# Kernel tuning notes

Hardware: AMD Instinct MI355X
Metric: run time of the kernel (lower is better)

The kernel has to match this reference:

```python
import jax, jax.numpy as jnp
import numpy as np
import math

H = 1024
N_HEADS = 16
B, S = 2, 2048

def setup_inputs() -> dict:
    key = jax.random.key(0)
    ks = jax.random.split(key, 10)
    s = 0.02
    inp = {
        "x": jax.random.normal(ks[0], (B, S, H), dtype=jnp.float32),
        "attention_mask": jnp.zeros((B, 1, 1, S), dtype=jnp.float32),
        "Wq": jax.random.normal(ks[1], (H, H), dtype=jnp.float32) * s,
        "bq": jnp.zeros((H,), dtype=jnp.float32),
        "Wk": jax.random.normal(ks[2], (H, H), dtype=jnp.float32) * s,
        "bk": jnp.zeros((H,), dtype=jnp.float32),
        "Wv": jax.random.normal(ks[3], (H, H), dtype=jnp.float32) * s,
        "bv": jnp.zeros((H,), dtype=jnp.float32),
        "Wo": jax.random.normal(ks[4], (H, H), dtype=jnp.float32) * s,
        "bo": jnp.zeros((H,), dtype=jnp.float32),
    }
    return inp

def reference(x, attention_mask, Wq, bq, Wk, bk, Wv, bv, Wo, bo):
    b, s, h = x.shape
    n = N_HEADS
    d = h // n
    scale = 1.0 / math.sqrt(h / n)
    # Linear projections (torch Linear: x @ W.T + b)
    q = (x @ Wq.T + bq).reshape(b, s, n, d).transpose(0, 2, 1, 3)  # [b,n,s,d]
    k = (x @ Wk.T + bk).reshape(b, s, n, d).transpose(0, 2, 1, 3)
    v = (x @ Wv.T + bv).reshape(b, s, n, d).transpose(0, 2, 1, 3)
    scores = jnp.einsum("bnqd,bnkd->bnqk", q, k) * scale + attention_mask
    probs = jax.nn.softmax(scores, axis=-1)
    attn = jnp.einsum("bnqk,bnkd->bnqd", probs, v)
    attn = attn.transpose(0, 2, 1, 3).reshape(b, s, h)
    return attn @ Wo.T + bo
```

## Files before the change

### kernel.cpp

```cpp
#include <hip/hip_runtime.h>

typedef __bf16 bf16;
typedef __bf16 bf16x8 __attribute__((ext_vector_type(8)));
typedef __bf16 bf16x4 __attribute__((ext_vector_type(4)));
typedef float f32x4 __attribute__((ext_vector_type(4)));
typedef unsigned int u32;
typedef const u32 __attribute__((address_space(1)))* gp1_t;
typedef u32 __attribute__((address_space(3)))* lp3_t;

constexpr int Hdim = 1024;
constexpr int SEQ  = 2048;
constexpr int NB   = 2;
constexpr int NHEAD = 16;
constexpr int DHEAD = 64;
constexpr int MR = NB * SEQ;
constexpr float LOG2E = 1.4426950408889634f;
constexpr float QSCALE = 0.125f * LOG2E;

__device__ __forceinline__ float fexp2(float x) { return __builtin_amdgcn_exp2f(x); }

__device__ __forceinline__ void gld16(const void* g, void* l) {
  __builtin_amdgcn_global_load_lds((gp1_t)g, (lp3_t)l, 16, 0, 0);
}

__global__ __launch_bounds__(256) void cvt_all_k(
    const float* __restrict__ x, const float* __restrict__ Wq, const float* __restrict__ Wk,
    const float* __restrict__ Wv, const float* __restrict__ Wo, const float* __restrict__ mask,
    bf16* __restrict__ xb, bf16* __restrict__ wqkv, bf16* __restrict__ wob,
    float* __restrict__ maskS) {
  const int n8x = MR * Hdim / 8;
  const int n8w = Hdim * Hdim / 8;
  int i = blockIdx.x * 256 + threadIdx.x;
  if (i >= n8x + 4 * n8w) {
    int o = i - (n8x + 4 * n8w);
    const float4* p = reinterpret_cast<const float4*>(mask) + (size_t)o * 2;
    float4 a = p[0], b = p[1];
    a.x *= LOG2E; a.y *= LOG2E; a.z *= LOG2E; a.w *= LOG2E;
    b.x *= LOG2E; b.y *= LOG2E; b.z *= LOG2E; b.w *= LOG2E;
    float4* q = reinterpret_cast<float4*>(maskS) + (size_t)o * 2;
    q[0] = a; q[1] = b;
    return;
  }
  const float* src;
  bf16* dst;
  int slot;
  if (i < n8x) {
    src = x; dst = xb; slot = i;
  } else {
    int j = i - n8x;
    int w = j >> 17;
    int o = j & (n8w - 1);
    if (w == 0)      { src = Wq; dst = wqkv;            }
    else if (w == 1) { src = Wk; dst = wqkv + (size_t)Hdim * Hdim;     }
    else if (w == 2) { src = Wv; dst = wqkv + (size_t)2 * Hdim * Hdim; }
    else             { src = Wo; dst = wob;             }
    slot = o;
  }
  const float4* p = reinterpret_cast<const float4*>(src) + (size_t)slot * 2;
  float4 a = p[0], b = p[1];
  bf16x8 o8;
  o8[0] = (bf16)a.x; o8[1] = (bf16)a.y; o8[2] = (bf16)a.z; o8[3] = (bf16)a.w;
  o8[4] = (bf16)b.x; o8[5] = (bf16)b.y; o8[6] = (bf16)b.z; o8[7] = (bf16)b.w;
  reinterpret_cast<bf16x8*>(dst)[slot] = o8;
}

__global__ __launch_bounds__(256) void qkv_gemm_k(
    const bf16* __restrict__ A, const bf16* __restrict__ Bw,
    const float* __restrict__ bq, const float* __restrict__ bk, const float* __restrict__ bv,
    bf16* __restrict__ Qw, bf16* __restrict__ Kw, bf16* __restrict__ VTw)
{
  __shared__ __align__(16) bf16 As[3][128][32];
  __shared__ __align__(16) bf16 Bs[3][128][32];

  const int t = threadIdx.x;
  const int lane = t & 63, wave = t >> 6;
  const int ql = lane & 15, g = lane >> 4;
  const int wr = wave >> 1, wc = wave & 1;
  const int row0 = blockIdx.x * 128;
  const int col0 = blockIdx.y * 128;
  const int z = blockIdx.y >> 3;
  const float* bias = (z == 0) ? bq : (z == 1) ? bk : bv;

  f32x4 acc[4][4] = {};

#define STAGE_QKV(buf, kt)                                                        \
  {                                                                               \
    _Pragma("unroll")                                                             \
    for (int i = 0; i < 2; ++i) {                                                 \
      int c = i * 256 + t;                                                        \
      int r = c >> 2, o = (c & 3) << 3;                                           \
      gld16(&A[(size_t)(row0 + r) * Hdim + (kt) + o], (char*)&As[buf][0][0] + c * 16); \
      gld16(&Bw[(size_t)(col0 + r) * Hdim + (kt) + o], (char*)&Bs[buf][0][0] + c * 16); \
    }                                                                             \
  }

  constexpr int NT = Hdim / 32;
  STAGE_QKV(0, 0);
  STAGE_QKV(1, 32);

  int cur = 0;
  for (int it = 0; it < NT; ++it) {
    if (it + 2 < NT) {
      int stg = cur + 2; if (stg >= 3) stg -= 3;
      STAGE_QKV(stg, (it + 2) * 32);
      asm volatile("s_waitcnt vmcnt(8)" ::: "memory");
    } else if (it + 1 < NT) {
      asm volatile("s_waitcnt vmcnt(4)" ::: "memory");
    } else {
      asm volatile("s_waitcnt vmcnt(0)" ::: "memory");
    }
    __builtin_amdgcn_s_barrier();

    bf16x8 af[4], bfr[4];
#pragma unroll
    for (int m = 0; m < 4; ++m)
      af[m] = *reinterpret_cast<const bf16x8*>(&As[cur][wr * 64 + m * 16 + ql][g * 8]);
#pragma unroll
    for (int n = 0; n < 4; ++n)
      bfr[n] = *reinterpret_cast<const bf16x8*>(&Bs[cur][wc * 64 + n * 16 + ql][g * 8]);
#pragma unroll
    for (int m = 0; m < 4; ++m)
#pragma unroll
      for (int n = 0; n < 4; ++n)
        acc[m][n] = __builtin_amdgcn_mfma_f32_16x16x32_bf16(af[m], bfr[n], acc[m][n], 0, 0, 0);

    __builtin_amdgcn_s_barrier();
    cur = (cur + 1 == 3) ? 0 : cur + 1;
  }
#undef STAGE_QKV

  const float oscale = (z == 0) ? QSCALE : 1.0f;
#pragma unroll
  for (int m = 0; m < 4; ++m) {
#pragma unroll
    for (int n = 0; n < 4; ++n) {
#pragma unroll
      for (int r = 0; r < 4; ++r) {
        int gi = row0 + wr * 64 + m * 16 + g * 4 + r;
        int gj = col0 + wc * 64 + n * 16 + ql;
        int j1 = gj & (Hdim - 1);
        float v = (acc[m][n][r] + bias[j1]) * oscale;
        int b = gi >> 11, s = gi & (SEQ - 1);
        int hh = j1 >> 6, dd = j1 & 63;
        if (z == 0)
          Qw[((size_t)(b * NHEAD + hh) * SEQ + s) * DHEAD + dd] = (bf16)v;
        else if (z == 1)
          Kw[((size_t)(b * NHEAD + hh) * SEQ + s) * DHEAD + dd] = (bf16)v;
        else
          VTw[((size_t)(b * NHEAD + hh) * DHEAD + dd) * SEQ + s] = (bf16)v;
      }
    }
  }
}

__global__ __launch_bounds__(256, 2) void attn_fwd_k(
    const bf16* __restrict__ Q, const bf16* __restrict__ K,
    const bf16* __restrict__ VT, const float* __restrict__ maskS,
    bf16* __restrict__ Out)
{
  const int head = blockIdx.x;
  const int qt = blockIdx.y;
  const int b = head >> 4;
  const int hh = head & 15;
  const int t = threadIdx.x, lane = t & 63, wave = t >> 6;
  const int ql = lane & 15, g = lane >> 4;
  const int swz = (ql & 7) << 4;

  __shared__ __align__(16) bf16 Ks[2][64][64];
  __shared__ __align__(16) bf16 VTs[2][64][64];
  __shared__ __align__(16) bf16 Ps[4][32][64];

  const bf16* Qh  = Q  + (size_t)head * SEQ * DHEAD;
  const bf16* Kh  = K  + (size_t)head * SEQ * DHEAD;
  const bf16* VTh = VT + (size_t)head * DHEAD * SEQ;
  const float* mrow = maskS + (size_t)b * SEQ;

  const int q0w = qt * 128 + wave * 32;
  char* psw = (char*)&Ps[wave][0][0];

  bf16x8 qf[2][2];
#pragma unroll
  for (int qm = 0; qm < 2; ++qm)
#pragma unroll
    for (int kk = 0; kk < 2; ++kk)
      qf[qm][kk] = *reinterpret_cast<const bf16x8*>(
          &Qh[(size_t)(q0w + qm * 16 + ql) * DHEAD + kk * 32 + g * 8]);

  f32x4 accT[2][4] = {};
  f32x4 psum4[2] = {{0.f, 0.f, 0.f, 0.f}, {0.f, 0.f, 0.f, 0.f}};

#pragma unroll
  for (int i = 0; i < 2; ++i) {
    int c = i * 256 + t, r = c >> 3, sp = c & 7, sl = sp ^ (r & 7);
    gld16(&Kh[(size_t)r * DHEAD + sl * 8], (char*)&Ks[0][0][0] + c * 16);
    gld16(&VTh[(size_t)r * SEQ + sl * 8], (char*)&VTs[0][0][0] + c * 16);
  }
  __syncthreads();

  for (int it = 0; it < SEQ / 64; ++it) {
    const int cur = it & 1;
    const int kb0 = it * 64;

    f32x4 mk4[4];
#pragma unroll
    for (int kb = 0; kb < 4; ++kb)
      mk4[kb] = *reinterpret_cast<const f32x4*>(mrow + kb0 + kb * 16 + g * 4);

    if (it + 1 < SEQ / 64) {
      const int nb0 = kb0 + 64;
#pragma unroll
      for (int i = 0; i < 2; ++i) {
        int c = i * 256 + t, r = c >> 3, sp = c & 7, sl = sp ^ (r & 7);
        gld16(&Kh[(size_t)(nb0 + r) * DHEAD + sl * 8], (char*)&Ks[cur ^ 1][0][0] + c * 16);
        gld16(&VTh[(size_t)r * SEQ + nb0 + sl * 8], (char*)&VTs[cur ^ 1][0][0] + c * 16);
      }
    }

    const char* ksb = (const char*)&Ks[cur][0][0];
    const char* vsb = (const char*)&VTs[cur][0][0];

    bf16x8 kf[4][2];
#pragma unroll
    for (int kb = 0; kb < 4; ++kb) {
      const int row = kb * 16 + ql;
#pragma unroll
      for (int kk = 0; kk < 2; ++kk)
        kf[kb][kk] = *reinterpret_cast<const bf16x8*>(ksb + row * 128 + ((kk * 64 + g * 16) ^ swz));
    }
    f32x4 sacc[2][4];
#pragma unroll
    for (int qm = 0; qm < 2; ++qm)
#pragma unroll
      for (int kb = 0; kb < 4; ++kb) sacc[qm][kb] = mk4[kb];
    __builtin_amdgcn_s_setprio(1);
#pragma unroll
    for (int qm = 0; qm < 2; ++qm)
#pragma unroll
      for (int kb = 0; kb < 4; ++kb)
#pragma unroll
        for (int kk = 0; kk < 2; ++kk)
          sacc[qm][kb] = __builtin_amdgcn_mfma_f32_16x16x32_bf16(kf[kb][kk], qf[qm][kk], sacc[qm][kb], 0, 0, 0);
    __builtin_amdgcn_s_setprio(0);

#pragma unroll
    for (int qm = 0; qm < 2; ++qm) {
      const int qrow = qm * 16 + ql;
#pragma unroll
      for (int kb = 0; kb < 2; ++kb) {
        bf16x4 p4;
        f32x4 pv;
#pragma unroll
        for (int r = 0; r < 4; ++r) { pv[r] = fexp2(sacc[qm][kb][r]); p4[r] = (bf16)pv[r]; }
        psum4[qm] += pv;
        *reinterpret_cast<bf16x4*>(psw + qrow * 128 + ((kb * 32 + g * 8) ^ swz)) = p4;
      }
    }

    bf16x8 vf[4][2];
#pragma unroll
    for (int db = 0; db < 4; ++db) {
      const int row = db * 16 + ql;
#pragma unroll
      for (int kk = 0; kk < 2; ++kk)
        vf[db][kk] = *reinterpret_cast<const bf16x8*>(vsb + row * 128 + ((kk * 64 + g * 16) ^ swz));
    }

    bf16x8 pf0[2];
#pragma unroll
    for (int qm = 0; qm < 2; ++qm)
      pf0[qm] = *reinterpret_cast<const bf16x8*>(psw + (qm * 16 + ql) * 128 + ((g * 16) ^ swz));
    __builtin_amdgcn_s_setprio(1);
#pragma unroll
    for (int qm = 0; qm < 2; ++qm)
#pragma unroll
      for (int db = 0; db < 4; ++db)
        accT[qm][db] = __builtin_amdgcn_mfma_f32_16x16x32_bf16(vf[db][0], pf0[qm], accT[qm][db], 0, 0, 0);
    __builtin_amdgcn_s_setprio(0);

#pragma unroll
    for (int qm = 0; qm < 2; ++qm) {
      const int qrow = qm * 16 + ql;
#pragma unroll
      for (int kb = 2; kb < 4; ++kb) {
        bf16x4 p4;
        f32x4 pv;
#pragma unroll
        for (int r = 0; r < 4; ++r) { pv[r] = fexp2(sacc[qm][kb][r]); p4[r] = (bf16)pv[r]; }
        psum4[qm] += pv;
        *reinterpret_cast<bf16x4*>(psw + qrow * 128 + ((kb * 32 + g * 8) ^ swz)) = p4;
      }
    }

    bf16x8 pf1[2];
#pragma unroll
    for (int qm = 0; qm < 2; ++qm)
      pf1[qm] = *reinterpret_cast<const bf16x8*>(psw + (qm * 16 + ql) * 128 + ((64 + g * 16) ^ swz));
    __builtin_amdgcn_s_setprio(1);
#pragma unroll
    for (int qm = 0; qm < 2; ++qm)
#pragma unroll
      for (int db = 0; db < 4; ++db)
        accT[qm][db] = __builtin_amdgcn_mfma_f32_16x16x32_bf16(vf[db][1], pf1[qm], accT[qm][db], 0, 0, 0);
    __builtin_amdgcn_s_setprio(0);

    __syncthreads();
  }

  asm volatile("s_waitcnt lgkmcnt(0)" ::: "memory");
#pragma unroll
  for (int qm = 0; qm < 2; ++qm) {
    float l = (psum4[qm][0] + psum4[qm][1]) + (psum4[qm][2] + psum4[qm][3]);
    l += __shfl_xor(l, 16);
    l += __shfl_xor(l, 32);
    const float inv = 1.0f / l;
    const int qrow = qm * 16 + ql;
#pragma unroll
    for (int db = 0; db < 4; ++db) {
      bf16x4 o4;
#pragma unroll
      for (int r = 0; r < 4; ++r) o4[r] = (bf16)(accT[qm][db][r] * inv);
      *reinterpret_cast<bf16x4*>(psw + qrow * 128 + ((db * 32 + g * 8) ^ swz)) = o4;
    }
  }
  asm volatile("s_waitcnt lgkmcnt(0)" ::: "memory");
#pragma unroll
  for (int i = 0; i < 4; ++i) {
    const int row = i * 8 + (lane >> 3);
    bf16x8 v = *reinterpret_cast<const bf16x8*>(psw + row * 128 + (((lane & 7) << 4) ^ ((row & 7) << 4)));
    *reinterpret_cast<bf16x8*>(&Out[((size_t)(b * SEQ) + q0w + row) * Hdim + hh * 64 + (lane & 7) * 8]) = v;
  }
}

__global__ __launch_bounds__(256) void out_gemm_k(
    const bf16* __restrict__ A, const bf16* __restrict__ Bm,
    const float* __restrict__ bias, float* __restrict__ C)
{
  __shared__ __align__(16) bf16 As[3][128][32];
  __shared__ __align__(16) bf16 Bs[3][64][32];

  const int t = threadIdx.x;
  const int lane = t & 63, wave = t >> 6;
  const int ql = lane & 15, g = lane >> 4;
  const int wr = wave >> 1, wc = wave & 1;
  const int row0 = blockIdx.x * 128;
  const int col0 = blockIdx.y * 64;

  f32x4 acc[4][2] = {};

#define STAGE_OUT(buf, kt)                                                        \
  {                                                                               \
    _Pragma("unroll")                                                             \
    for (int i = 0; i < 2; ++i) {                                                 \
      int c = i * 256 + t;                                                        \
      int r = c >> 2, o = (c & 3) << 3;                                           \
      gld16(&A[(size_t)(row0 + r) * Hdim + (kt) + o], (char*)&As[buf][0][0] + c * 16); \
    }                                                                             \
    {                                                                             \
      int c = t;                                                                  \
      int r = c >> 2, o = (c & 3) << 3;                                           \
      gld16(&Bm[(size_t)(col0 + r) * Hdim + (kt) + o], (char*)&Bs[buf][0][0] + c * 16); \
    }                                                                             \
  }

  constexpr int NT = Hdim / 32;
  STAGE_OUT(0, 0);
  STAGE_OUT(1, 32);

  int cur = 0;
  for (int it = 0; it < NT; ++it) {
    if (it + 2 < NT) {
      int stg = cur + 2; if (stg >= 3) stg -= 3;
      STAGE_OUT(stg, (it + 2) * 32);
      asm volatile("s_waitcnt vmcnt(6)" ::: "memory");
    } else if (it + 1 < NT) {
      asm volatile("s_waitcnt vmcnt(3)" ::: "memory");
    } else {
      asm volatile("s_waitcnt vmcnt(0)" ::: "memory");
    }
    __builtin_amdgcn_s_barrier();

    bf16x8 af[4], bfr[2];
#pragma unroll
    for (int m = 0; m < 4; ++m)
      af[m] = *reinterpret_cast<const bf16x8*>(&As[cur][wr * 64 + m * 16 + ql][g * 8]);
#pragma unroll
    for (int n = 0; n < 2; ++n)
      bfr[n] = *reinterpret_cast<const bf16x8*>(&Bs[cur][wc * 32 + n * 16 + ql][g * 8]);
#pragma unroll
    for (int m = 0; m < 4; ++m)
#pragma unroll
      for (int n = 0; n < 2; ++n)
        acc[m][n] = __builtin_amdgcn_mfma_f32_16x16x32_bf16(af[m], bfr[n], acc[m][n], 0, 0, 0);

    __builtin_amdgcn_s_barrier();
    cur = (cur + 1 == 3) ? 0 : cur + 1;
  }
#undef STAGE_OUT

#pragma unroll
  for (int m = 0; m < 4; ++m)
#pragma unroll
    for (int n = 0; n < 2; ++n)
#pragma unroll
      for (int r = 0; r < 4; ++r) {
        int gi = row0 + wr * 64 + m * 16 + g * 4 + r;
        int gj = col0 + wc * 32 + n * 16 + ql;
        C[(size_t)gi * Hdim + gj] = acc[m][n][r] + bias[gj];
      }
}

extern "C" void kernel_launch(void* const* d_in, const int* in_sizes, int n_in,
                              void* d_out, int out_size, void* d_ws, size_t ws_size,
                              hipStream_t stream) {
  const float* x    = (const float*)d_in[0];
  const float* mask = (const float*)d_in[1];
  const float* Wq   = (const float*)d_in[2];
  const float* bq   = (const float*)d_in[3];
  const float* Wk   = (const float*)d_in[4];
  const float* bk   = (const float*)d_in[5];
  const float* Wv   = (const float*)d_in[6];
  const float* bv   = (const float*)d_in[7];
  const float* Wo   = (const float*)d_in[8];
  const float* bo   = (const float*)d_in[9];
  float* out = (float*)d_out;

  bf16* xb   = (bf16*)d_ws;
  const size_t big = (size_t)MR * Hdim;
  bf16* wqkv = xb + big;
  bf16* wob  = wqkv + (size_t)3 * Hdim * Hdim;
  bf16* qw   = wob + (size_t)Hdim * Hdim;
  bf16* kw   = qw + big;
  bf16* vtw  = kw + big;
  bf16* attnb = vtw + big;
  float* maskS = (float*)(attnb + big);

  const int nslots = MR * Hdim / 8 + 4 * (Hdim * Hdim / 8) + NB * SEQ / 8;
  cvt_all_k<<<nslots / 256, 256, 0, stream>>>(x, Wq, Wk, Wv, Wo, mask, xb, wqkv, wob, maskS);

  qkv_gemm_k<<<dim3(MR / 128, 3 * Hdim / 128), 256, 0, stream>>>(
      xb, wqkv, bq, bk, bv, qw, kw, vtw);

  attn_fwd_k<<<dim3(NB * NHEAD, SEQ / 128), 256, 0, stream>>>(qw, kw, vtw, maskS, attnb);

  out_gemm_k<<<dim3(MR / 128, Hdim / 64), 256, 0, stream>>>(attnb, wob, bo, out);
}
```

Baseline: 122.5 us.

## Switch attention to 32x32x16 MFMA with register-resident P via permlane32 swap

Rewrites the attention inner loop to use 32x32x16 bf16 MFMA tiles instead of 16x16x32. The probability tile now stays in registers: it is packed with v_cvt_pk_bf16_f32 and rearranged with v_permlane32_swap, which removes the per-wave P shared-memory buffer and its LDS round trip. The output staging reuses the K buffer. The freed LDS allows raising the occupancy hint to 3 blocks per CU. The risks are higher register pressure at the new occupancy and correctness of the lane permutation and the staging reuse.

```diff
diff --git a/kernel.cpp b/kernel.cpp
--- a/kernel.cpp
+++ b/kernel.cpp
@@ -4,7 +4,9 @@
 typedef __bf16 bf16x8 __attribute__((ext_vector_type(8)));
 typedef __bf16 bf16x4 __attribute__((ext_vector_type(4)));
 typedef float f32x4 __attribute__((ext_vector_type(4)));
+typedef float f32x16 __attribute__((ext_vector_type(16)));
 typedef unsigned int u32;
+typedef u32 u32x4 __attribute__((ext_vector_type(4)));
 typedef const u32 __attribute__((address_space(1)))* gp1_t;
 typedef u32 __attribute__((address_space(3)))* lp3_t;
 
@@ -21,6 +23,12 @@
 
 __device__ __forceinline__ void gld16(const void* g, void* l) {
   __builtin_amdgcn_global_load_lds((gp1_t)g, (lp3_t)l, 16, 0, 0);
+}
+
+__device__ __forceinline__ u32 cvtpk_bf16(float lo, float hi) {
+  u32 r;
+  asm("v_cvt_pk_bf16_f32 %0, %1, %2" : "=v"(r) : "v"(lo), "v"(hi));
+  return r;
 }
 
 __global__ __launch_bounds__(256) void cvt_all_k(
@@ -153,7 +161,7 @@
   }
 }
 
-__global__ __launch_bounds__(256, 2) void attn_fwd_k(
+__global__ __launch_bounds__(256, 3) void attn_fwd_k(
     const bf16* __restrict__ Q, const bf16* __restrict__ K,
     const bf16* __restrict__ VT, const float* __restrict__ maskS,
     bf16* __restrict__ Out)
@@ -163,12 +171,10 @@
   const int b = head >> 4;
   const int hh = head & 15;
   const int t = threadIdx.x, lane = t & 63, wave = t >> 6;
-  const int ql = lane & 15, g = lane >> 4;
-  const int swz = (ql & 7) << 4;
+  const int q = lane & 31, h = lane >> 5;
 
   __shared__ __align__(16) bf16 Ks[2][64][64];
   __shared__ __align__(16) bf16 VTs[2][64][64];
-  __shared__ __align__(16) bf16 Ps[4][32][64];
 
   const bf16* Qh  = Q  + (size_t)head * SEQ * DHEAD;
   const bf16* Kh  = K  + (size_t)head * SEQ * DHEAD;
@@ -176,18 +182,14 @@
   const float* mrow = maskS + (size_t)b * SEQ;
 
   const int q0w = qt * 128 + wave * 32;
-  char* psw = (char*)&Ps[wave][0][0];
-
-  bf16x8 qf[2][2];
-#pragma unroll
-  for (int qm = 0; qm < 2; ++qm)
-#pragma unroll
-    for (int kk = 0; kk < 2; ++kk)
-      qf[qm][kk] = *reinterpret_cast<const bf16x8*>(
-          &Qh[(size_t)(q0w + qm * 16 + ql) * DHEAD + kk * 32 + g * 8]);
-
-  f32x4 accT[2][4] = {};
-  f32x4 psum4[2] = {{0.f, 0.f, 0.f, 0.f}, {0.f, 0.f, 0.f, 0.f}};
+
+  bf16x8 qf[4];
+#pragma unroll
+  for (int s = 0; s < 4; ++s)
+    qf[s] = *reinterpret_cast<const bf16x8*>(&Qh[(size_t)(q0w + q) * DHEAD + s * 16 + 8 * h]);
+
+  f32x16 accT[2] = {};
+  f32x4 psum4 = {0.f, 0.f, 0.f, 0.f};
 
 #pragma unroll
   for (int i = 0; i < 2; ++i) {
@@ -201,11 +203,6 @@
     const int cur = it & 1;
     const int kb0 = it * 64;
 
-    f32x4 mk4[4];
-#pragma unroll
-    for (int kb = 0; kb < 4; ++kb)
-      mk4[kb] = *reinterpret_cast<const f32x4*>(mrow + kb0 + kb * 16 + g * 4);
-
     if (it + 1 < SEQ / 64) {
       const int nb0 = kb0 + 64;
 #pragma unroll
@@ -219,114 +216,89 @@
     const char* ksb = (const char*)&Ks[cur][0][0];
     const char* vsb = (const char*)&VTs[cur][0][0];
 
-    bf16x8 kf[4][2];
-#pragma unroll
-    for (int kb = 0; kb < 4; ++kb) {
-      const int row = kb * 16 + ql;
-#pragma unroll
-      for (int kk = 0; kk < 2; ++kk)
-        kf[kb][kk] = *reinterpret_cast<const bf16x8*>(ksb + row * 128 + ((kk * 64 + g * 16) ^ swz));
-    }
-    f32x4 sacc[2][4];
-#pragma unroll
-    for (int qm = 0; qm < 2; ++qm)
-#pragma unroll
-      for (int kb = 0; kb < 4; ++kb) sacc[qm][kb] = mk4[kb];
+    f32x16 sacc[2];
+#pragma unroll
+    for (int tt = 0; tt < 2; ++tt) {
+#pragma unroll
+      for (int s = 0; s < 4; ++s) {
+        f32x4 m4 = *reinterpret_cast<const f32x4*>(mrow + kb0 + 32 * tt + 8 * s + 4 * h);
+#pragma unroll
+        for (int r = 0; r < 4; ++r) sacc[tt][s * 4 + r] = m4[r];
+      }
+    }
+
     __builtin_amdgcn_s_setprio(1);
 #pragma unroll
-    for (int qm = 0; qm < 2; ++qm)
-#pragma unroll
-      for (int kb = 0; kb < 4; ++kb)
-#pragma unroll
-        for (int kk = 0; kk < 2; ++kk)
-          sacc[qm][kb] = __builtin_amdgcn_mfma_f32_16x16x32_bf16(kf[kb][kk], qf[qm][kk], sacc[qm][kb], 0, 0, 0);
+    for (int tt = 0; tt < 2; ++tt) {
+      const int row = 32 * tt + q;
+      const int rsw = (row & 7) << 4;
+#pragma unroll
+      for (int s = 0; s < 4; ++s) {
+        bf16x8 kf = *reinterpret_cast<const bf16x8*>(ksb + row * 128 + ((32 * s + 16 * h) ^ rsw));
+        sacc[tt] = __builtin_amdgcn_mfma_f32_32x32x16_bf16(kf, qf[s], sacc[tt], 0, 0, 0);
+      }
+    }
     __builtin_amdgcn_s_setprio(0);
 
-#pragma unroll
-    for (int qm = 0; qm < 2; ++qm) {
-      const int qrow = qm * 16 + ql;
-#pragma unroll
-      for (int kb = 0; kb < 2; ++kb) {
-        bf16x4 p4;
-        f32x4 pv;
-#pragma unroll
-        for (int r = 0; r < 4; ++r) { pv[r] = fexp2(sacc[qm][kb][r]); p4[r] = (bf16)pv[r]; }
-        psum4[qm] += pv;
-        *reinterpret_cast<bf16x4*>(psw + qrow * 128 + ((kb * 32 + g * 8) ^ swz)) = p4;
-      }
-    }
-
-    bf16x8 vf[4][2];
-#pragma unroll
-    for (int db = 0; db < 4; ++db) {
-      const int row = db * 16 + ql;
-#pragma unroll
-      for (int kk = 0; kk < 2; ++kk)
-        vf[db][kk] = *reinterpret_cast<const bf16x8*>(vsb + row * 128 + ((kk * 64 + g * 16) ^ swz));
-    }
-
-    bf16x8 pf0[2];
-#pragma unroll
-    for (int qm = 0; qm < 2; ++qm)
-      pf0[qm] = *reinterpret_cast<const bf16x8*>(psw + (qm * 16 + ql) * 128 + ((g * 16) ^ swz));
+    float pe[2][16];
+#pragma unroll
+    for (int tt = 0; tt < 2; ++tt)
+#pragma unroll
+      for (int i = 0; i < 16; ++i) {
+        pe[tt][i] = fexp2(sacc[tt][i]);
+        psum4[i & 3] += pe[tt][i];
+      }
+
+    u32x4 pw[4];
+#pragma unroll
+    for (int m = 0; m < 4; ++m) {
+      const int tt = m >> 1, mi = (m & 1) * 8;
+      u32 w0a = cvtpk_bf16(pe[tt][mi + 0], pe[tt][mi + 1]);
+      u32 w0b = cvtpk_bf16(pe[tt][mi + 2], pe[tt][mi + 3]);
+      u32 w1a = cvtpk_bf16(pe[tt][mi + 4], pe[tt][mi + 5]);
+      u32 w1b = cvtpk_bf16(pe[tt][mi + 6], pe[tt][mi + 7]);
+      asm("v_permlane32_swap_b32 %0, %1" : "+v"(w0a), "+v"(w1a));
+      asm("v_permlane32_swap_b32 %0, %1" : "+v"(w0b), "+v"(w1b));
+      pw[m][0] = w0a; pw[m][1] = w0b; pw[m][2] = w1a; pw[m][3] = w1b;
+    }
+
     __builtin_amdgcn_s_setprio(1);
 #pragma unroll
-    for (int qm = 0; qm < 2; ++qm)
-#pragma unroll
-      for (int db = 0; db < 4; ++db)
-        accT[qm][db] = __builtin_amdgcn_mfma_f32_16x16x32_bf16(vf[db][0], pf0[qm], accT[qm][db], 0, 0, 0);
+    for (int td = 0; td < 2; ++td) {
+      const int row = 32 * td + q;
+      const int rsw = (row & 7) << 4;
+#pragma unroll
+      for (int m = 0; m < 4; ++m) {
+        bf16x8 vf = *reinterpret_cast<const bf16x8*>(vsb + row * 128 + ((32 * m + 16 * h) ^ rsw));
+        bf16x8 pf = __builtin_bit_cast(bf16x8, pw[m]);
+        accT[td] = __builtin_amdgcn_mfma_f32_32x32x16_bf16(vf, pf, accT[td], 0, 0, 0);
+      }
+    }
     __builtin_amdgcn_s_setprio(0);
 
-#pragma unroll
-    for (int qm = 0; qm < 2; ++qm) {
-      const int qrow = qm * 16 + ql;
-#pragma unroll
-      for (int kb = 2; kb < 4; ++kb) {
-        bf16x4 p4;
-        f32x4 pv;
-#pragma unroll
-        for (int r = 0; r < 4; ++r) { pv[r] = fexp2(sacc[qm][kb][r]); p4[r] = (bf16)pv[r]; }
-        psum4[qm] += pv;
-        *reinterpret_cast<bf16x4*>(psw + qrow * 128 + ((kb * 32 + g * 8) ^ swz)) = p4;
-      }
-    }
-
-    bf16x8 pf1[2];
-#pragma unroll
-    for (int qm = 0; qm < 2; ++qm)
-      pf1[qm] = *reinterpret_cast<const bf16x8*>(psw + (qm * 16 + ql) * 128 + ((64 + g * 16) ^ swz));
-    __builtin_amdgcn_s_setprio(1);
-#pragma unroll
-    for (int qm = 0; qm < 2; ++qm)
-#pragma unroll
-      for (int db = 0; db < 4; ++db)
-        accT[qm][db] = __builtin_amdgcn_mfma_f32_16x16x32_bf16(vf[db][1], pf1[qm], accT[qm][db], 0, 0, 0);
-    __builtin_amdgcn_s_setprio(0);
-
     __syncthreads();
   }
 
-  asm volatile("s_waitcnt lgkmcnt(0)" ::: "memory");
-#pragma unroll
-  for (int qm = 0; qm < 2; ++qm) {
-    float l = (psum4[qm][0] + psum4[qm][1]) + (psum4[qm][2] + psum4[qm][3]);
-    l += __shfl_xor(l, 16);
-    l += __shfl_xor(l, 32);
-    const float inv = 1.0f / l;
-    const int qrow = qm * 16 + ql;
-#pragma unroll
-    for (int db = 0; db < 4; ++db) {
+  float l = (psum4[0] + psum4[1]) + (psum4[2] + psum4[3]);
+  l += __shfl_xor(l, 32);
+  const float inv = 1.0f / l;
+
+  char* slab = (char*)&Ks[0][0][0] + wave * 4096;
+  const int qsw = (q & 7) << 4;
+#pragma unroll
+  for (int td = 0; td < 2; ++td)
+#pragma unroll
+    for (int s = 0; s < 4; ++s) {
       bf16x4 o4;
 #pragma unroll
-      for (int r = 0; r < 4; ++r) o4[r] = (bf16)(accT[qm][db][r] * inv);
-      *reinterpret_cast<bf16x4*>(psw + qrow * 128 + ((db * 32 + g * 8) ^ swz)) = o4;
-    }
-  }
+      for (int r = 0; r < 4; ++r) o4[r] = (bf16)(accT[td][s * 4 + r] * inv);
+      *reinterpret_cast<bf16x4*>(slab + q * 128 + (((32 * td + 8 * s + 4 * h) * 2) ^ qsw)) = o4;
+    }
   asm volatile("s_waitcnt lgkmcnt(0)" ::: "memory");
 #pragma unroll
   for (int i = 0; i < 4; ++i) {
     const int row = i * 8 + (lane >> 3);
-    bf16x8 v = *reinterpret_cast<const bf16x8*>(psw + row * 128 + (((lane & 7) << 4) ^ ((row & 7) << 4)));
+    bf16x8 v = *reinterpret_cast<const bf16x8*>(slab + row * 128 + (((lane & 7) << 4) ^ ((row & 7) << 4)));
     *reinterpret_cast<bf16x8*>(&Out[((size_t)(b * SEQ) + q0w + row) * Hdim + hh * 64 + (lane & 7) * 8]) = v;
   }
 }
```

Result: no change. 123.0 us (+0.4%).
